# Optimization experiments

Hardware: AMD Instinct MI355X
Metric: run time of the kernel (lower is better)

## Reference

```python
import jax, jax.numpy as jnp
import numpy as np

B, S, C = 1, 2048, 2048
H, D = 16, 128
FF = 8192
EPS = 1e-6


def _rms(x, w):
    return x * jax.lax.rsqrt(jnp.mean(x * x, axis=-1, keepdims=True) + EPS) * w


def _rope(x, cos, sin):
    # x: [B,S,H,D]; cos/sin: [S,D]
    x1, x2 = jnp.split(x, 2, axis=-1)
    rot = jnp.concatenate([-x2, x1], axis=-1)
    return x * cos[None, :, None, :] + rot * sin[None, :, None, :]


def setup_inputs() -> dict:
    key = jax.random.key(0)
    ks = jax.random.split(key, 12)
    # RoPE tables
    inv_freq = 1.0 / (10000.0 ** (jnp.arange(0, D, 2, dtype=jnp.float32) / D))
    freqs = jnp.arange(S, dtype=jnp.float32)[:, None] * inv_freq[None, :]
    emb = jnp.concatenate([freqs, freqs], axis=-1)  # [S,D]
    # causal additive mask
    causal = jnp.tril(jnp.ones((S, S), dtype=bool))
    mask = jnp.where(causal, 0.0, -1e9).astype(jnp.float32)[None, None]
    w = lambda k, shp: (jax.random.normal(k, shp, dtype=jnp.float32) * 0.02)
    return {
        "hidden_states": jax.random.normal(ks[0], (B, S, C), dtype=jnp.float32),
        "cos": jnp.cos(emb),
        "sin": jnp.sin(emb),
        "attention_mask": mask,
        "ln1_w": jnp.ones((C,), dtype=jnp.float32),
        "wq": w(ks[1], (C, C)),
        "wk": w(ks[2], (C, C)),
        "wv": w(ks[3], (C, C)),
        "wo": w(ks[4], (C, C)),
        "ln2_w": jnp.ones((C,), dtype=jnp.float32),
        "w_gate": w(ks[5], (FF, C)),
        "w_up": w(ks[6], (FF, C)),
        "w_down": w(ks[7], (C, FF)),
    }


def reference(hidden_states, cos, sin, attention_mask, ln1_w, wq, wk, wv, wo,
              ln2_w, w_gate, w_up, w_down):
    # --- input RMSNorm ---
    x = _rms(hidden_states, ln1_w)
    # --- W2 (Gaussian-kernel) attention ---
    q = (x @ wq.T).reshape(B, S, H, D)
    k = (x @ wk.T).reshape(B, S, H, D)
    v = (x @ wv.T).reshape(B, S, H, D)
    q = _rope(q, cos, sin).transpose(0, 2, 1, 3)  # [B,H,S,D]
    k = _rope(k, cos, sin).transpose(0, 2, 1, 3)
    v = v.transpose(0, 2, 1, 3)
    qk = jnp.einsum('bhid,bhjd->bhij', q, k)
    q2 = jnp.sum(q * q, axis=-1)  # [B,H,S]
    k2 = jnp.sum(k * k, axis=-1)
    dist2 = q2[..., :, None] - 2.0 * qk + k2[..., None, :]  # ||q-k||^2
    scores = -dist2 / (2.0 * np.sqrt(D).astype(np.float32)) + attention_mask
    attn = jax.nn.softmax(scores, axis=-1)
    ctx = jnp.einsum('bhij,bhjd->bhid', attn, v)
    attn_out = ctx.transpose(0, 2, 1, 3).reshape(B, S, C) @ wo.T
    h = hidden_states + attn_out
    # --- post-attn RMSNorm + SwiGLU FFN ---
    y = _rms(h, ln2_w)
    ffn = (jax.nn.silu(y @ w_gate.T) * (y @ w_up.T)) @ w_down.T
    return h + ffn
```

## Files before the change

### kernel.cpp

```cpp
#include <hip/hip_runtime.h>
#include <cstdint>
#include <cstddef>

typedef __bf16 bf16x8 __attribute__((ext_vector_type(8)));
typedef float f32x4 __attribute__((ext_vector_type(4)));

union V16 { uint4 u; bf16x8 b; unsigned short s[8]; };

__device__ __forceinline__ float b2f(unsigned short u) {
  unsigned int x = ((unsigned int)u) << 16;
  float f;
  __builtin_memcpy(&f, &x, 4);
  return f;
}
__device__ __forceinline__ unsigned short f2b(float f) {
  unsigned int u;
  __builtin_memcpy(&u, &f, 4);
  u = u + 0x7FFFu + ((u >> 16) & 1u);
  return (unsigned short)(u >> 16);
}

__device__ __forceinline__ f32x4 mfma16(bf16x8 a, bf16x8 b, f32x4 c) {
  return __builtin_amdgcn_mfma_f32_16x16x32_bf16(a, b, c, 0, 0, 0);
}

__device__ __forceinline__ void gld_lds16(const unsigned short* g, unsigned short* l) {
  __builtin_amdgcn_global_load_lds((__attribute__((address_space(1))) void*)g,
                                   (__attribute__((address_space(3))) void*)l,
                                   16, 0, 0);
}

__global__ __launch_bounds__(256) void cvt_all(const float* __restrict__ wq,
                                               const float* __restrict__ wk,
                                               const float* __restrict__ wv,
                                               const float* __restrict__ wo,
                                               const float* __restrict__ wg,
                                               const float* __restrict__ wu,
                                               const float* __restrict__ wd,
                                               unsigned short* __restrict__ dst) {
  const int b = blockIdx.x;
  const float* src;
  if (b < 16384) {
    const int w = b >> 12;
    src = (w == 0 ? wq : w == 1 ? wk : w == 2 ? wv : wo) + (size_t)(b & 4095) * 1024;
  } else if (b < 32768) {
    src = wg + (size_t)(b - 16384) * 1024;
  } else if (b < 49152) {
    src = wu + (size_t)(b - 32768) * 1024;
  } else {
    src = wd + (size_t)(b - 49152) * 1024;
  }
  const int o = threadIdx.x * 4;
  const float4 v = *(const float4*)(src + o);
  ushort4 r;
  r.x = f2b(v.x); r.y = f2b(v.y); r.z = f2b(v.z); r.w = f2b(v.w);
  *(ushort4*)(dst + (size_t)b * 1024 + o) = r;
}

__global__ __launch_bounds__(256) void rms_k(const float* __restrict__ xin,
                                             const float* __restrict__ wgt,
                                             unsigned short* __restrict__ out) {
  const int s = blockIdx.x;
  const int t = threadIdx.x;
  float vals[8];
  float ss = 0.f;
#pragma unroll
  for (int i = 0; i < 8; ++i) {
    const int c = t + i * 256;
    const float f = xin[(size_t)s * 2048 + c];
    vals[i] = f;
    ss += f * f;
  }
#pragma unroll
  for (int off = 32; off > 0; off >>= 1) ss += __shfl_xor(ss, off);
  __shared__ float red[4];
  if ((t & 63) == 0) red[t >> 6] = ss;
  __syncthreads();
  ss = red[0] + red[1] + red[2] + red[3];
  const float sc = rsqrtf(ss * (1.f / 2048.f) + 1e-6f);
#pragma unroll
  for (int i = 0; i < 8; ++i) {
    const int c = t + i * 256;
    out[(size_t)s * 2048 + c] = f2b(vals[i] * sc * wgt[c]);
  }
}

__global__ __launch_bounds__(256) void rope_qk(unsigned short* qb, unsigned short* kb,
                                               const float* __restrict__ cosb,
                                               const float* __restrict__ sinb,
                                               float* __restrict__ k2c) {
  const int idx = blockIdx.x * 256 + threadIdx.x;
  const int d = idx & 63;
  const int h = (idx >> 6) & 15;
  const int s = idx >> 10;
  const size_t base = (size_t)s * 2048 + h * 128;
  const int cb = s * 128;
  const float c1 = cosb[cb + d],      s1 = sinb[cb + d];
  const float c2 = cosb[cb + d + 64], s2 = sinb[cb + d + 64];
  {
    const float x1 = b2f(qb[base + d]), x2 = b2f(qb[base + d + 64]);
    qb[base + d]      = f2b(x1 * c1 - x2 * s1);
    qb[base + d + 64] = f2b(x2 * c2 + x1 * s2);
  }
  {
    const float x1 = b2f(kb[base + d]), x2 = b2f(kb[base + d + 64]);
    const float k1 = x1 * c1 - x2 * s1;
    const float k2 = x2 * c2 + x1 * s2;
    kb[base + d]      = f2b(k1);
    kb[base + d + 64] = f2b(k2);
    float ss = k1 * k1 + k2 * k2;
#pragma unroll
    for (int off = 32; off > 0; off >>= 1) ss += __shfl_xor(ss, off);
    if (d == 0) k2c[h * 2048 + s] = ss * 0.04419417382415922f;
  }
}

template <int EPI, int RT>
__global__ __launch_bounds__(256, 2) void gemm_nt(
    const unsigned short* __restrict__ A,
    const unsigned short* __restrict__ B0,
    const unsigned short* __restrict__ B1,
    const unsigned short* __restrict__ B2,
    unsigned short* C0, unsigned short* C1, unsigned short* C2,
    const float* auxf, float* Cf,
    int N, int K, int kstride) {
  constexpr int TM = RT * 32;
  constexpr int APASS = TM / 64;
  const unsigned short* B;
  unsigned short* C;
  size_t koff = 0;
  if constexpr (EPI == 0) {
    B = (blockIdx.z == 0) ? B0 : (blockIdx.z == 1 ? B1 : B2);
    C = (blockIdx.z == 0) ? C0 : (blockIdx.z == 1 ? C1 : C2);
  } else {
    B = B0;
    C = C0;
    if constexpr (EPI == 3) koff = (size_t)blockIdx.z * K;
  }

  const int m0 = blockIdx.y * TM;
  const int n0 = blockIdx.x * 128;
  const int t = threadIdx.x;
  const int lane = t & 63;
  const int w = t >> 6;
  const int quad = lane >> 4;
  const int l15 = lane & 15;
  const int wr = w >> 1;
  const int wc = w & 1;

  __shared__ __align__(16) unsigned short As[TM * 32];
  __shared__ __align__(16) unsigned short Bs[128 * 32];

  const f32x4 vzero = {0.f, 0.f, 0.f, 0.f};
  f32x4 acc[RT][4];
#pragma unroll
  for (int i = 0; i < RT; ++i)
#pragma unroll
    for (int j = 0; j < 4; ++j) acc[i][j] = vzero;

  const int srow = w * 16 + (lane >> 2);
  const int scol = (lane & 3) * 8;
  const unsigned short* Ag = A + (size_t)(m0 + srow) * kstride + scol + koff;
  const unsigned short* Bg = B + (size_t)(n0 + srow) * kstride + scol + koff;

  for (int k0 = 0; k0 < K; k0 += 32) {
#pragma unroll
    for (int p = 0; p < APASS; ++p)
      gld_lds16(Ag + (size_t)p * 64 * kstride + k0, As + p * 2048 + w * 512);
#pragma unroll
    for (int p = 0; p < 2; ++p)
      gld_lds16(Bg + (size_t)p * 64 * kstride + k0, Bs + p * 2048 + w * 512);
    __syncthreads();

    bf16x8 af[RT], bfr[4];
#pragma unroll
    for (int rt = 0; rt < RT; ++rt)
      af[rt] = *(const bf16x8*)&As[(wr * (RT * 16) + rt * 16 + l15) * 32 + quad * 8];
#pragma unroll
    for (int ct = 0; ct < 4; ++ct)
      bfr[ct] = *(const bf16x8*)&Bs[(wc * 64 + ct * 16 + l15) * 32 + quad * 8];
#pragma unroll
    for (int rt = 0; rt < RT; ++rt)
#pragma unroll
      for (int ct = 0; ct < 4; ++ct)
        acc[rt][ct] = mfma16(af[rt], bfr[ct], acc[rt][ct]);
    __syncthreads();
  }

  float* Cfz = Cf;
  if constexpr (EPI == 3)
    Cfz = Cf + (size_t)blockIdx.z * (size_t)gridDim.y * TM * N;

#pragma unroll
  for (int rt = 0; rt < RT; ++rt) {
#pragma unroll
    for (int ct = 0; ct < 4; ++ct) {
#pragma unroll
      for (int r = 0; r < 4; ++r) {
        const int m = m0 + wr * (RT * 16) + rt * 16 + quad * 4 + r;
        const int n = n0 + wc * 64 + ct * 16 + l15;
        const size_t idx = (size_t)m * N + n;
        const float a = acc[rt][ct][r];
        if constexpr (EPI == 0) {
          C[idx] = f2b(a);
        } else if constexpr (EPI == 1) {
          Cf[idx] = auxf[idx] + a;
        } else {
          Cfz[idx] = a;
        }
      }
    }
  }
}

#define BARRIER() asm volatile("s_barrier" ::: "memory")
#define WAITVM(N) asm volatile("s_waitcnt vmcnt(" #N ")" ::: "memory")
#define WAITLG()                                           \
  do {                                                     \
    asm volatile("s_waitcnt lgkmcnt(0)" ::: "memory");     \
    __builtin_amdgcn_sched_barrier(0);                     \
  } while (0)

#define LOADA(APT, MQ)                                                         \
  _Pragma("unroll") for (int j = 0; j < 4; ++j)                                \
  _Pragma("unroll") for (int ks = 0; ks < 2; ++ks)                             \
      afr[j][ks] = *(const bf16x8*)((APT) + ((MQ) * 64 + j * 16 + l15) * 64 +  \
                                    (ks ? ko1 : ko0));

#define LOADB(BPT, NQ)                                                         \
  _Pragma("unroll") for (int jn = 0; jn < 2; ++jn)                             \
  _Pragma("unroll") for (int ks = 0; ks < 2; ++ks)                             \
      bfr[(NQ) * 2 + jn][ks] =                                                 \
          *(const bf16x8*)((BPT) + ((NQ) * 32 + jn * 16 + l15) * 64 +          \
                           (ks ? ko1 : ko0));

#define MFMAQ(MQ, NQ)                                                          \
  do {                                                                         \
    __builtin_amdgcn_s_setprio(1);                                             \
    _Pragma("unroll") for (int j = 0; j < 4; ++j)                              \
    _Pragma("unroll") for (int jn = 0; jn < 2; ++jn)                           \
    _Pragma("unroll") for (int ks = 0; ks < 2; ++ks)                           \
        acc[(MQ) * 4 + j][(NQ) * 2 + jn] =                                     \
            mfma16(afr[j][ks], bfr[(NQ) * 2 + jn][ks],                         \
                   acc[(MQ) * 4 + j][(NQ) * 2 + jn]);                          \
    __builtin_amdgcn_s_setprio(0);                                             \
  } while (0)

#define STAGE8(DA, DB)                                                         \
  do {                                                                         \
    _Pragma("unroll") for (int h = 0; h < 2; ++h)                              \
    _Pragma("unroll") for (int i = 0; i < 2; ++i) {                            \
      gld_lds16(sAg + (size_t)(h * 128 + i * 64) * kstr,                       \
                (DA) + h * 8192 + i * 4096 + w * 512);                         \
      gld_lds16(sBg + (size_t)(h * 128 + i * 64) * kstr,                       \
                (DB) + h * 8192 + i * 4096 + w * 512);                         \
    }                                                                          \
    sAg += 64;                                                                 \
    sBg += 64;                                                                 \
  } while (0)

#define TILEGRP(APT, BPT, STG, WTB)                                            \
  do {                                                                         \
    LOADA(APT, 0);                                                             \
    LOADB(BPT, 0);                                                             \
    BARRIER(); WAITLG(); MFMAQ(0, 0); BARRIER();                               \
    LOADB(BPT, 1);                                                             \
    BARRIER(); WAITLG(); MFMAQ(0, 1); BARRIER();                               \
    LOADA(APT, 1);                                                             \
    BARRIER(); WAITLG(); MFMAQ(1, 0); BARRIER();                               \
    STG;                                                                       \
    BARRIER(); MFMAQ(1, 1); WTB; BARRIER();                                    \
  } while (0)

template <int EPI>
__global__ __launch_bounds__(512, 2) void gemm256(
    const unsigned short* __restrict__ A,
    const unsigned short* __restrict__ B,
    unsigned short* __restrict__ C0,
    unsigned short* __restrict__ C1,
    unsigned short* __restrict__ C2,
    float* __restrict__ Cf,
    int N, int kstr, int Ktiles) {
  const int gx = gridDim.x, gy = gridDim.y;
  const int nwg = gx * gy * gridDim.z;
  const int orig = blockIdx.x + gx * (blockIdx.y + gy * blockIdx.z);
  const int s = ((nwg & 7) == 0) ? ((orig & 7) * (nwg >> 3) + (orig >> 3)) : orig;
  const int bx = s % gx;
  const int sq = s / gx;
  const int by = sq % gy;
  const int bz = sq / gy;

  const int m0 = by * 256, n0 = bx * 256;
  const size_t koff = (size_t)bz * ((size_t)Ktiles * 64);

  const int t = threadIdx.x;
  const int lane = t & 63;
  const int w = t >> 6;
  const int quad = lane >> 4;
  const int l15 = lane & 15;
  const int wr = w >> 2;
  const int wc = w & 3;

  __shared__ __align__(16) unsigned short As[2][2][8192];
  __shared__ __align__(16) unsigned short Bs[2][2][8192];

  const f32x4 vzero = {0.f, 0.f, 0.f, 0.f};
  f32x4 acc[8][4];
#pragma unroll
  for (int i = 0; i < 8; ++i)
#pragma unroll
    for (int j = 0; j < 4; ++j) acc[i][j] = vzero;

  bf16x8 afr[4][2], bfr[4][2];

  const int lr = lane >> 3;
  const int lc = ((lane & 7) ^ lr) * 8;
  const unsigned short* sAg = A + (size_t)(m0 + w * 8 + lr) * kstr + koff + lc;
  const unsigned short* sBg = B + (size_t)(n0 + w * 8 + lr) * kstr + koff + lc;

  unsigned short* Asb0 = &As[0][0][0];
  unsigned short* Asb1 = &As[1][0][0];
  unsigned short* Bsb0 = &Bs[0][0][0];
  unsigned short* Bsb1 = &Bs[1][0][0];
  const unsigned short* Aw0 = &As[0][wr][0];
  const unsigned short* Aw1 = &As[1][wr][0];
  const unsigned short* Bw0 = &Bs[0][wc >> 1][0] + (wc & 1) * 4096;
  const unsigned short* Bw1 = &Bs[1][wc >> 1][0] + (wc & 1) * 4096;

  const int ax = (l15 & 7) * 8;
  const int ko0 = (quad * 8) ^ ax;
  const int ko1 = (32 + quad * 8) ^ ax;

  STAGE8(Asb0, Bsb0);
  STAGE8(Asb1, Bsb1);
  WAITVM(8);
  BARRIER();

  const int nIter = (Ktiles >> 1) - 1;
  for (int it = 0; it < nIter; ++it) {
    TILEGRP(Aw0, Bw0, STAGE8(Asb0, Bsb0), WAITVM(8));
    TILEGRP(Aw1, Bw1, STAGE8(Asb1, Bsb1), WAITVM(8));
  }
  TILEGRP(Aw0, Bw0, (void)0, WAITVM(0));
  TILEGRP(Aw1, Bw1, (void)0, (void)0);

  if constexpr (EPI == 2) {
    const size_t MN = (size_t)gy * 256 * N;
    float* Cp = Cf + (size_t)bz * MN;
#pragma unroll
    for (int mf = 0; mf < 8; ++mf) {
      const int m = m0 + wr * 128 + mf * 16 + quad * 4;
#pragma unroll
      for (int nf = 0; nf < 4; ++nf) {
        const int n = n0 + wc * 64 + nf * 16 + l15;
#pragma unroll
        for (int r = 0; r < 4; ++r) Cp[(size_t)(m + r) * N + n] = acc[mf][nf][r];
      }
    }
  } else {
    unsigned short* Cp;
    int nb;
    constexpr int ldc = (EPI == 0) ? 8192 : 2048;
    if constexpr (EPI == 0) {
      Cp = (n0 < 8192) ? C0 : C1;
      nb = n0 & 8191;
    } else {
      const int wsel = n0 >> 11;
      Cp = wsel == 0 ? C0 : (wsel == 1 ? C1 : C2);
      nb = n0 & 2047;
    }
#pragma unroll
    for (int mf = 0; mf < 8; ++mf) {
      const int m = m0 + wr * 128 + mf * 16 + quad * 4;
#pragma unroll
      for (int nf = 0; nf < 4; ++nf) {
        const int n = nb + wc * 64 + nf * 16 + l15;
#pragma unroll
        for (int r = 0; r < 4; ++r)
          Cp[(size_t)(m + r) * ldc + n] = f2b(acc[mf][nf][r]);
      }
    }
  }
}

__global__ __launch_bounds__(256) void silu_k(unsigned short* __restrict__ g,
                                              const unsigned short* __restrict__ u) {
  const size_t i = ((size_t)blockIdx.x * 256 + threadIdx.x) * 8;
  V16 gv, uv, ov;
  gv.u = *(const uint4*)(g + i);
  uv.u = *(const uint4*)(u + i);
#pragma unroll
  for (int e = 0; e < 8; ++e) {
    const float gf = b2f(gv.s[e]);
    const float uf = b2f(uv.s[e]);
    ov.s[e] = f2b(gf / (1.f + __expf(-gf)) * uf);
  }
  *(uint4*)(g + i) = ov.u;
}

__global__ __launch_bounds__(256) void comb4(const float* __restrict__ p,
                                             const float* __restrict__ hf,
                                             float* __restrict__ out) {
  const size_t i = ((size_t)blockIdx.x * 256 + threadIdx.x) * 4;
  const size_t MN = (size_t)2048 * 2048;
  float4 a = *(const float4*)(p + i);
  const float4 b = *(const float4*)(p + MN + i);
  const float4 c = *(const float4*)(p + 2 * MN + i);
  const float4 d = *(const float4*)(p + 3 * MN + i);
  const float4 h = *(const float4*)(hf + i);
  a.x += b.x + c.x + d.x + h.x;
  a.y += b.y + c.y + d.y + h.y;
  a.z += b.z + c.z + d.z + h.z;
  a.w += b.w + c.w + d.w + h.w;
  *(float4*)(out + i) = a;
}

__global__ __launch_bounds__(256, 3) void flash_w2(
    const unsigned short* __restrict__ q,
    const unsigned short* __restrict__ kk,
    const unsigned short* __restrict__ v,
    const float* __restrict__ k2c,
    unsigned short* __restrict__ ctx) {
  constexpr int Cw = 2048;
  constexpr float TWOC = 0.08838834764831843f;
  const int h = blockIdx.y;
  const int i = (h >= 8) ? (31 - blockIdx.x) : blockIdx.x;
  const int i0 = i * 64;
  const int t = threadIdx.x;
  const int lane = t & 63;
  const int w = t >> 6;
  const int quad = lane >> 4;
  const int l15 = lane & 15;

  __shared__ __align__(16) unsigned short Ks[64 * 136];
  __shared__ __align__(16) unsigned short VTs[128 * 72];
  __shared__ __align__(16) unsigned short Ps[4][16 * 72];

  bf16x8 aq[4];
  {
    const unsigned short* qp = q + (size_t)(i0 + w * 16 + l15) * Cw + h * 128;
#pragma unroll
    for (int kt = 0; kt < 4; ++kt) {
      V16 u;
      u.u = *(const uint4*)(qp + kt * 32 + quad * 8);
      aq[kt] = u.b;
    }
  }

  const f32x4 vzero = {0.f, 0.f, 0.f, 0.f};
  f32x4 o[8];
#pragma unroll
  for (int nt = 0; nt < 8; ++nt) o[nt] = vzero;
  float mrow[4] = {-1e30f, -1e30f, -1e30f, -1e30f};
  float lrow[4] = {0.f, 0.f, 0.f, 0.f};

  const int njt = i + 1;
  const int jr = t >> 2;
  const int c0 = (t & 3) * 32;
  const int jlo = jr & 7;
  const int jhi = jr >> 3;
  for (int jt = 0; jt < njt; ++jt) {
    const int j0 = jt * 64;
    __syncthreads();
    {
      const unsigned short* kp = kk + (size_t)(j0 + jr) * Cw + h * 128 + c0;
      const unsigned short* vp = v + (size_t)(j0 + jr) * Cw + h * 128 + c0;
#pragma unroll
      for (int ii = 0; ii < 4; ++ii) {
        *(uint4*)&Ks[jr * 136 + c0 + ii * 8] = *(const uint4*)(kp + ii * 8);
        V16 vu;
        vu.u = *(const uint4*)(vp + ii * 8);
#pragma unroll
        for (int e = 0; e < 8; ++e) {
          const int dd = c0 + ii * 8 + e;
          const int gs = (jhi ^ (dd >> 4)) & 7;
          VTs[dd * 72 + (jlo | (gs << 3))] = vu.s[e];
        }
      }
    }
    __syncthreads();

    float k2v[4];
#pragma unroll
    for (int ct = 0; ct < 4; ++ct) k2v[ct] = k2c[h * 2048 + j0 + ct * 16 + l15];

    f32x4 sc[4];
#pragma unroll
    for (int ct = 0; ct < 4; ++ct) {
      f32x4 a = vzero;
#pragma unroll
      for (int kt = 0; kt < 4; ++kt) {
        V16 u;
        u.u = *(const uint4*)&Ks[(ct * 16 + l15) * 136 + kt * 32 + quad * 8];
        a = mfma16(aq[kt], u.b, a);
      }
      sc[ct] = a;
    }

    const bool diag = (jt == njt - 1);
#pragma unroll
    for (int ct = 0; ct < 4; ++ct) {
#pragma unroll
      for (int r = 0; r < 4; ++r) {
        float s = fmaf(TWOC, sc[ct][r], -k2v[ct]);
        if (diag) {
          const int gi = w * 16 + quad * 4 + r;
          const int gj = ct * 16 + l15;
          s = (gj <= gi) ? s : -1e30f;
        }
        sc[ct][r] = s;
      }
    }

    float al[4];
#pragma unroll
    for (int r = 0; r < 4; ++r) {
      float rm = fmaxf(fmaxf(sc[0][r], sc[1][r]), fmaxf(sc[2][r], sc[3][r]));
      rm = fmaxf(rm, __shfl_xor(rm, 1));
      rm = fmaxf(rm, __shfl_xor(rm, 2));
      rm = fmaxf(rm, __shfl_xor(rm, 4));
      rm = fmaxf(rm, __shfl_xor(rm, 8));
      const float mn = fmaxf(mrow[r], rm);
      al[r] = __expf(mrow[r] - mn);
      mrow[r] = mn;
      float ps = 0.f;
#pragma unroll
      for (int ct = 0; ct < 4; ++ct) {
        const float p = __expf(sc[ct][r] - mn);
        sc[ct][r] = p;
        ps += p;
      }
      ps += __shfl_xor(ps, 1);
      ps += __shfl_xor(ps, 2);
      ps += __shfl_xor(ps, 4);
      ps += __shfl_xor(ps, 8);
      lrow[r] = lrow[r] * al[r] + ps;
    }
#pragma unroll
    for (int nt = 0; nt < 8; ++nt)
#pragma unroll
      for (int r = 0; r < 4; ++r) o[nt][r] *= al[r];

#pragma unroll
    for (int ct = 0; ct < 4; ++ct)
#pragma unroll
      for (int r = 0; r < 4; ++r)
        Ps[w][(quad * 4 + r) * 72 + ct * 16 + l15] = f2b(sc[ct][r]);

#pragma unroll
    for (int kt2 = 0; kt2 < 2; ++kt2) {
      V16 pa;
      pa.u = *(const uint4*)&Ps[w][l15 * 72 + kt2 * 32 + quad * 8];
#pragma unroll
      for (int nt = 0; nt < 8; ++nt) {
        V16 vb;
        const int dd = nt * 16 + l15;
        const int gs = (kt2 * 4 + quad) ^ nt;
        vb.u = *(const uint4*)&VTs[dd * 72 + gs * 8];
        o[nt] = mfma16(pa.b, vb.b, o[nt]);
      }
    }
  }

  float invl[4];
#pragma unroll
  for (int r = 0; r < 4; ++r) invl[r] = 1.f / lrow[r];
#pragma unroll
  for (int nt = 0; nt < 8; ++nt) {
#pragma unroll
    for (int r = 0; r < 4; ++r) {
      const int gi = i0 + w * 16 + quad * 4 + r;
      ctx[(size_t)gi * Cw + h * 128 + nt * 16 + l15] = f2b(o[nt][r] * invl[r]);
    }
  }
}

extern "C" void kernel_launch(void* const* d_in, const int* in_sizes, int n_in,
                              void* d_out, int out_size, void* d_ws, size_t ws_size,
                              hipStream_t stream) {
  (void)in_sizes; (void)n_in; (void)out_size; (void)ws_size;
  const float* hid  = (const float*)d_in[0];
  const float* cosb = (const float*)d_in[1];
  const float* sinb = (const float*)d_in[2];
  const float* ln1w = (const float*)d_in[4];
  const float* wq   = (const float*)d_in[5];
  const float* wk   = (const float*)d_in[6];
  const float* wv   = (const float*)d_in[7];
  const float* wo   = (const float*)d_in[8];
  const float* ln2w = (const float*)d_in[9];
  const float* wg   = (const float*)d_in[10];
  const float* wu   = (const float*)d_in[11];
  const float* wd   = (const float*)d_in[12];
  float* outp = (float*)d_out;

  const size_t SC = (size_t)2048 * 2048;
  const size_t FC = (size_t)8192 * 2048;
  unsigned short* p = (unsigned short*)d_ws;
  unsigned short* wqb = p;  p += SC;
  unsigned short* wkb = p;  p += SC;
  unsigned short* wvb = p;  p += SC;
  unsigned short* wob = p;  p += SC;
  unsigned short* wgb = p;  p += FC;
  unsigned short* wub = p;  p += FC;
  unsigned short* wdb = p;  p += FC;
  unsigned short* xn  = p;  p += SC;
  unsigned short* qb  = p;  p += SC;
  unsigned short* kb  = p;  p += SC;
  unsigned short* vb  = p;  p += SC;
  unsigned short* ctxb = p; p += SC;
  float* hf = (float*)p;   p += 2 * SC;
  float* k2cb = (float*)p;
  unsigned short* yn = xn;
  unsigned short* gate = wqb;
  unsigned short* upb  = qb;
  float* pd = (float*)wgb;

  cvt_all<<<65536, 256, 0, stream>>>(wq, wk, wv, wo, wg, wu, wd, wqb);

  rms_k<<<2048, 256, 0, stream>>>(hid, ln1w, xn);
  gemm256<1><<<dim3(24, 8, 1), 512, 0, stream>>>(xn, wqb, qb, kb, vb, nullptr,
                                                 6144, 2048, 32);
  rope_qk<<<8192, 256, 0, stream>>>(qb, kb, cosb, sinb, k2cb);
  flash_w2<<<dim3(32, 16), 256, 0, stream>>>(qb, kb, vb, k2cb, ctxb);
  gemm_nt<1, 2><<<dim3(16, 32, 1), 256, 0, stream>>>(ctxb, wob, wob, wob,
                                                     nullptr, nullptr, nullptr,
                                                     hid, hf, 2048, 2048, 2048);
  rms_k<<<2048, 256, 0, stream>>>(hf, ln2w, yn);
  gemm256<0><<<dim3(64, 8, 1), 512, 0, stream>>>(yn, wgb, gate, upb, nullptr, nullptr,
                                                 16384, 2048, 32);
  silu_k<<<8192, 256, 0, stream>>>(gate, upb);
  gemm256<2><<<dim3(8, 8, 4), 512, 0, stream>>>(gate, wdb, nullptr, nullptr, nullptr,
                                                pd, 2048, 8192, 32);
  comb4<<<4096, 256, 0, stream>>>(pd, hf, outp);
}
```

Baseline: 825.6 us.

## Restructure GEMM main loop into half-K stages with finer-grained prefetch

Reworks the 256x256 GEMM mainloop so each 64-wide K tile is split into two 32-wide halves with separate LDS slots. Global-to-LDS loads for A and B are issued interleaved with MFMA phases, and a new swizzle replaces the previous XOR scheme. The aim is to spread memory traffic across the loop and keep more stages in flight, hiding load latency behind MFMA work. In exchange it adds more barriers and vmcnt waits per tile, and the hand-written prologue and epilogue are intricate and easy to get wrong.

```diff
diff --git a/kernel.cpp b/kernel.cpp
--- a/kernel.cpp
+++ b/kernel.cpp
@@ -221,55 +221,51 @@
     __builtin_amdgcn_sched_barrier(0);                     \
   } while (0)
 
-#define LOADA(APT, MQ)                                                         \
+#define LDA(BUF, KS, MQ)                                                       \
   _Pragma("unroll") for (int j = 0; j < 4; ++j)                                \
-  _Pragma("unroll") for (int ks = 0; ks < 2; ++ks)                             \
-      afr[j][ks] = *(const bf16x8*)((APT) + ((MQ) * 64 + j * 16 + l15) * 64 +  \
-                                    (ks ? ko1 : ko0));
-
-#define LOADB(BPT, NQ)                                                         \
-  _Pragma("unroll") for (int jn = 0; jn < 2; ++jn)                             \
-  _Pragma("unroll") for (int ks = 0; ks < 2; ++ks)                             \
-      bfr[(NQ) * 2 + jn][ks] =                                                 \
-          *(const bf16x8*)((BPT) + ((NQ) * 32 + jn * 16 + l15) * 64 +          \
-                           (ks ? ko1 : ko0));
-
-#define MFMAQ(MQ, NQ)                                                          \
+      afr[j] = *(const bf16x8*)(aB + (BUF) * 16384 + (KS) * 8192 +             \
+                                ((MQ) * 64 + j * 16) * 32);
+
+#define LDB(BUF, KS)                                                           \
+  _Pragma("unroll") for (int nf = 0; nf < 4; ++nf)                             \
+      bfr[nf] = *(const bf16x8*)(bB + (BUF) * 16384 + (KS) * 8192 +            \
+                                 (nf * 16) * 32);
+
+#define MF(MQ)                                                                 \
   do {                                                                         \
     __builtin_amdgcn_s_setprio(1);                                             \
     _Pragma("unroll") for (int j = 0; j < 4; ++j)                              \
-    _Pragma("unroll") for (int jn = 0; jn < 2; ++jn)                           \
-    _Pragma("unroll") for (int ks = 0; ks < 2; ++ks)                           \
-        acc[(MQ) * 4 + j][(NQ) * 2 + jn] =                                     \
-            mfma16(afr[j][ks], bfr[(NQ) * 2 + jn][ks],                         \
-                   acc[(MQ) * 4 + j][(NQ) * 2 + jn]);                          \
+    _Pragma("unroll") for (int nf = 0; nf < 4; ++nf)                           \
+        acc[(MQ) * 4 + j][nf] = mfma16(afr[j], bfr[nf], acc[(MQ) * 4 + j][nf]);\
     __builtin_amdgcn_s_setprio(0);                                             \
   } while (0)
 
-#define STAGE8(DA, DB)                                                         \
+#define STA(BUF, KS)                                                           \
   do {                                                                         \
-    _Pragma("unroll") for (int h = 0; h < 2; ++h)                              \
-    _Pragma("unroll") for (int i = 0; i < 2; ++i) {                            \
-      gld_lds16(sAg + (size_t)(h * 128 + i * 64) * kstr,                       \
-                (DA) + h * 8192 + i * 4096 + w * 512);                         \
-      gld_lds16(sBg + (size_t)(h * 128 + i * 64) * kstr,                       \
-                (DB) + h * 8192 + i * 4096 + w * 512);                         \
-    }                                                                          \
-    sAg += 64;                                                                 \
-    sBg += 64;                                                                 \
+    unsigned short* d_ = AsB + (BUF) * 16384 + (KS) * 8192 + w * 512;          \
+    gld_lds16(pA, d_);                                                         \
+    gld_lds16(pA + (size_t)128 * kstr, d_ + 4096);                             \
+    pA += 32;                                                                  \
   } while (0)
 
-#define TILEGRP(APT, BPT, STG, WTB)                                            \
+#define STB(BUF, KS)                                                           \
   do {                                                                         \
-    LOADA(APT, 0);                                                             \
-    LOADB(BPT, 0);                                                             \
-    BARRIER(); WAITLG(); MFMAQ(0, 0); BARRIER();                               \
-    LOADB(BPT, 1);                                                             \
-    BARRIER(); WAITLG(); MFMAQ(0, 1); BARRIER();                               \
-    LOADA(APT, 1);                                                             \
-    BARRIER(); WAITLG(); MFMAQ(1, 0); BARRIER();                               \
-    STG;                                                                       \
-    BARRIER(); MFMAQ(1, 1); WTB; BARRIER();                                    \
+    unsigned short* d_ = BsB + (BUF) * 16384 + (KS) * 8192 + w * 512;          \
+    gld_lds16(pB, d_);                                                         \
+    gld_lds16(pB + (size_t)128 * kstr, d_ + 4096);                             \
+    pB += 32;                                                                  \
+  } while (0)
+
+#define TILE_STEADY(P)                                                         \
+  do {                                                                         \
+    LDA(P, 0, 0); LDB(P, 0); STA((P) ^ 1, 1);                                  \
+    BARRIER(); WAITLG(); MF(0); BARRIER();                                     \
+    LDA(P, 0, 1);            STB((P) ^ 1, 1);                                  \
+    BARRIER(); WAITLG(); MF(1); WAITVM(8); BARRIER();                          \
+    LDA(P, 1, 0); LDB(P, 1); STA(P, 0);                                        \
+    BARRIER(); WAITLG(); MF(0); BARRIER();                                     \
+    LDA(P, 1, 1);            STB(P, 0);                                        \
+    BARRIER(); WAITLG(); MF(1); WAITVM(8); BARRIER();                          \
   } while (0)
 
 template <int EPI>
@@ -303,6 +299,8 @@
 
   __shared__ __align__(16) unsigned short As[2][2][8192];
   __shared__ __align__(16) unsigned short Bs[2][2][8192];
+  unsigned short* AsB = &As[0][0][0];
+  unsigned short* BsB = &Bs[0][0][0];
 
   const f32x4 vzero = {0.f, 0.f, 0.f, 0.f};
   f32x4 acc[8][4];
@@ -311,38 +309,45 @@
 #pragma unroll
     for (int j = 0; j < 4; ++j) acc[i][j] = vzero;
 
-  bf16x8 afr[4][2], bfr[4][2];
-
-  const int lr = lane >> 3;
-  const int lc = ((lane & 7) ^ lr) * 8;
-  const unsigned short* sAg = A + (size_t)(m0 + w * 8 + lr) * kstr + koff + lc;
-  const unsigned short* sBg = B + (size_t)(n0 + w * 8 + lr) * kstr + koff + lc;
-
-  unsigned short* Asb0 = &As[0][0][0];
-  unsigned short* Asb1 = &As[1][0][0];
-  unsigned short* Bsb0 = &Bs[0][0][0];
-  unsigned short* Bsb1 = &Bs[1][0][0];
-  const unsigned short* Aw0 = &As[0][wr][0];
-  const unsigned short* Aw1 = &As[1][wr][0];
-  const unsigned short* Bw0 = &Bs[0][wc >> 1][0] + (wc & 1) * 4096;
-  const unsigned short* Bw1 = &Bs[1][wc >> 1][0] + (wc & 1) * 4096;
-
-  const int ax = (l15 & 7) * 8;
-  const int ko0 = (quad * 8) ^ ax;
-  const int ko1 = (32 + quad * 8) ^ ax;
-
-  STAGE8(Asb0, Bsb0);
-  STAGE8(Asb1, Bsb1);
+  bf16x8 afr[4], bfr[4];
+
+  const int ko = (quad ^ ((l15 >> 1) & 3)) * 8;
+  const unsigned short* aB = AsB + wr * 4096 + l15 * 32 + ko;
+  const unsigned short* bB = BsB + wc * 2048 + l15 * 32 + ko;
+
+  const int usrc = (lane & 3) ^ ((lane >> 3) & 3);
+  const unsigned short* pA =
+      A + (size_t)(m0 + w * 16 + (lane >> 2)) * kstr + koff + usrc * 8;
+  const unsigned short* pB =
+      B + (size_t)(n0 + w * 16 + (lane >> 2)) * kstr + koff + usrc * 8;
+
+  STA(0, 0); STB(0, 0);
+  STA(0, 1); STB(0, 1);
+  STA(1, 0); STB(1, 0);
   WAITVM(8);
   BARRIER();
 
-  const int nIter = (Ktiles >> 1) - 1;
-  for (int it = 0; it < nIter; ++it) {
-    TILEGRP(Aw0, Bw0, STAGE8(Asb0, Bsb0), WAITVM(8));
-    TILEGRP(Aw1, Bw1, STAGE8(Asb1, Bsb1), WAITVM(8));
-  }
-  TILEGRP(Aw0, Bw0, (void)0, WAITVM(0));
-  TILEGRP(Aw1, Bw1, (void)0, (void)0);
+  const int pairs = (Ktiles - 2) >> 1;
+  for (int it = 0; it < pairs; ++it) {
+    TILE_STEADY(0);
+    TILE_STEADY(1);
+  }
+  LDA(0, 0, 0); LDB(0, 0); STA(1, 1);
+  BARRIER(); WAITLG(); MF(0); BARRIER();
+  LDA(0, 0, 1);            STB(1, 1);
+  BARRIER(); WAITLG(); MF(1); WAITVM(8); BARRIER();
+  LDA(0, 1, 0); LDB(0, 1);
+  BARRIER(); WAITLG(); MF(0); BARRIER();
+  LDA(0, 1, 1);
+  BARRIER(); WAITLG(); MF(1); WAITVM(4); BARRIER();
+  LDA(1, 0, 0); LDB(1, 0);
+  BARRIER(); WAITLG(); MF(0); BARRIER();
+  LDA(1, 0, 1);
+  BARRIER(); WAITLG(); MF(1); WAITVM(0); BARRIER();
+  LDA(1, 1, 0); LDB(1, 1);
+  BARRIER(); WAITLG(); MF(0); BARRIER();
+  LDA(1, 1, 1);
+  BARRIER(); WAITLG(); MF(1);
 
   if constexpr (EPI == 2) {
     const size_t MN = (size_t)gy * 256 * N;
```

Result: faster. 763.8 us (-7.5%).
